# Kernel optimization log

Measured on AMD Instinct MI355X. Metric: run time of the kernel, lower is better.

## Reference

```python
import jax, jax.numpy as jnp
import numpy as np

N, E = 50000, 800000
D_IN, D_HID, D_OUT = 128, 128, 64
BN_EPS = 1e-5
GEN_EPS = 1e-7


def _lin_init(k, fan_in, shape):
    lim = 1.0 / np.sqrt(fan_in)
    return jax.random.uniform(k, shape, minval=-lim, maxval=lim, dtype=jnp.float32)


def setup_inputs() -> dict:
    key = jax.random.key(0)
    ks = jax.random.split(key, 12)
    x = jax.random.normal(ks[0], (N, D_IN), dtype=jnp.float32)
    edge_index = jax.random.randint(ks[1], (2, E), 0, N, dtype=jnp.int64)
    return {
        "x": x,
        # GCNConv 0 and 1 (Glorot-ish uniform init like PyG Linear)
        "W0": _lin_init(ks[2], D_IN, (D_IN, D_HID)), "b0": jnp.zeros((D_HID,), jnp.float32),
        "g0": jnp.ones((D_HID,), jnp.float32), "beta0": jnp.zeros((D_HID,), jnp.float32),
        "W1": _lin_init(ks[3], D_HID, (D_HID, D_HID)), "b1": jnp.zeros((D_HID,), jnp.float32),
        "g1": jnp.ones((D_HID,), jnp.float32), "beta1": jnp.zeros((D_HID,), jnp.float32),
        # GENConv MLP: [D_HID] -> [2*D_HID] (BN+ReLU) -> [D_OUT]
        "Wg1": _lin_init(ks[4], D_HID, (D_HID, 2 * D_HID)), "bg1": jnp.zeros((2 * D_HID,), jnp.float32),
        "gg": jnp.ones((2 * D_HID,), jnp.float32), "betag": jnp.zeros((2 * D_HID,), jnp.float32),
        "Wg2": _lin_init(ks[5], 2 * D_HID, (2 * D_HID, D_OUT)), "bg2": jnp.zeros((D_OUT,), jnp.float32),
        "edge_index": edge_index,
    }


def _bn(h, gamma, beta):
    # BatchNorm1d, training-mode batch statistics (biased variance)
    mu = jnp.mean(h, axis=0)
    var = jnp.mean(jnp.square(h - mu), axis=0)
    return (h - mu) * jax.lax.rsqrt(var + BN_EPS) * gamma + beta


def _gcn_conv(x, W, b, src, dst, n):
    # GCNConv: D^-1/2 (A + I) D^-1/2 (x W) + b
    loop = jnp.arange(n, dtype=src.dtype)
    s = jnp.concatenate([src, loop])
    d = jnp.concatenate([dst, loop])
    deg = jax.ops.segment_sum(jnp.ones_like(s, dtype=x.dtype), d, num_segments=n)
    dinv = jax.lax.rsqrt(deg)  # deg >= 1 due to self-loops
    norm = dinv[s] * dinv[d]   # [E+N]
    h = x @ W                  # [N, D]
    agg = jax.ops.segment_sum(norm[:, None] * h[s], d, num_segments=n)
    return agg + b


def _gen_conv(x, W1, b1, g, beta, W2, b2, src, dst, n):
    # GENConv (defaults): msg = relu(x_j) + eps; per-channel softmax aggregation
    # (t=1); residual add of x_dst; then MLP [D, 2D (BN+ReLU), D_out].
    msg = jax.nn.relu(x[src]) + GEN_EPS            # [E, D]
    m = jax.ops.segment_max(msg, dst, num_segments=n)
    m = jnp.where(jnp.isfinite(m), m, 0.0)         # guard zero in-degree nodes
    ex = jnp.exp(msg - m[dst])                     # [E, D]
    denom = jax.ops.segment_sum(ex, dst, num_segments=n)
    num = jax.ops.segment_sum(ex * msg, dst, num_segments=n)
    agg = num / jnp.maximum(denom, 1e-16)          # [N, D]
    out = agg + x                                  # residual
    h = jax.nn.relu(_bn(out @ W1 + b1, g, beta))
    return h @ W2 + b2


def reference(x, W0, b0, g0, beta0, W1, b1, g1, beta1,
              Wg1, bg1, gg, betag, Wg2, bg2, edge_index):
    src, dst = edge_index[0], edge_index[1]
    n = x.shape[0]
    # layer 0: GCNConv -> BN -> ReLU (dropout is identity in eval)
    h = _gcn_conv(x, W0, b0, src, dst, n)
    h = jax.nn.relu(_bn(h, g0, beta0))
    # layer 1
    h = _gcn_conv(h, W1, b1, src, dst, n)
    h = jax.nn.relu(_bn(h, g1, beta1))
    # final GENConv + log-softmax over classes
    h = _gen_conv(h, Wg1, bg1, gg, betag, Wg2, bg2, src, dst, n)
    return jax.nn.log_softmax(h, axis=-1)
```

## Files before the change

kernel.cpp:

```cpp
#include <hip/hip_runtime.h>
#include <hip/hip_bf16.h>

#define DIN 128
#define DHID 128
#define DCLS 64
#define BN_EPS 1e-5f
#define GEN_EPS 1e-7f

typedef __attribute__((ext_vector_type(8))) short short8;
typedef __attribute__((ext_vector_type(4))) float f32x4;

static __device__ __forceinline__ float bf2f(unsigned short u) {
    union { float f; unsigned int i; } x; x.i = ((unsigned int)u) << 16; return x.f;
}
static __device__ __forceinline__ unsigned short f2bf(float f) {
    union { float f; unsigned int i; } x; x.f = f;
    unsigned int r = x.i + 0x7fffu + ((x.i >> 16) & 1u);
    return (unsigned short)(r >> 16);
}
static __device__ __forceinline__ float bflo(unsigned int u) {
    union { float f; unsigned int i; } x; x.i = u << 16; return x.f;
}
static __device__ __forceinline__ float bfhi(unsigned int u) {
    union { float f; unsigned int i; } x; x.i = u & 0xffff0000u; return x.f;
}
static __device__ __forceinline__ unsigned int packbf(float lo, float hi) {
    return ((unsigned int)f2bf(hi) << 16) | f2bf(lo);
}

__global__ void k_hist(const int* __restrict__ dst, int* __restrict__ counts, int E) {
    int e = blockIdx.x * 256 + threadIdx.x;
    if (e < E) atomicAdd(&counts[dst[e]], 1);
}

__global__ __launch_bounds__(256) void k_scan1(const int* __restrict__ counts,
        int* __restrict__ roff, int* __restrict__ bsum, int N) {
    __shared__ int ls[256];
    int t = threadIdx.x;
    int base = blockIdx.x * 1024 + t * 4;
    int c0 = 0, c1 = 0, c2 = 0, c3 = 0;
    if (base + 3 < N) {
        int4 v = *(const int4*)(counts + base);
        c0 = v.x; c1 = v.y; c2 = v.z; c3 = v.w;
    } else {
        if (base + 0 < N) c0 = counts[base + 0];
        if (base + 1 < N) c1 = counts[base + 1];
        if (base + 2 < N) c2 = counts[base + 2];
        if (base + 3 < N) c3 = counts[base + 3];
    }
    ls[t] = c0 + c1 + c2 + c3;
    __syncthreads();
    for (int off = 1; off < 256; off <<= 1) {
        int v = (t >= off) ? ls[t - off] : 0;
        __syncthreads();
        ls[t] += v;
        __syncthreads();
    }
    int r = (t == 0) ? 0 : ls[t - 1];
    if (base + 0 < N) { roff[base + 0] = r; r += c0; }
    if (base + 1 < N) { roff[base + 1] = r; r += c1; }
    if (base + 2 < N) { roff[base + 2] = r; r += c2; }
    if (base + 3 < N) { roff[base + 3] = r; }
    if (t == 255) bsum[blockIdx.x] = ls[255];
}

__global__ void k_scan3(const int* __restrict__ counts, const int* __restrict__ bsum,
        int* __restrict__ roff, int* __restrict__ cursor, float* __restrict__ dinv,
        int N, int E) {
    __shared__ int sbase;
    if (threadIdx.x == 0) {
        int blk = (blockIdx.x * 256) >> 10;
        int s = 0;
        for (int j = 0; j < blk; j++) s += bsum[j];
        sbase = s;
    }
    __syncthreads();
    int i = blockIdx.x * 256 + threadIdx.x;
    if (i < N) {
        int r = roff[i] + sbase;
        roff[i] = r; cursor[i] = r;
        dinv[i] = rsqrtf((float)(counts[i] + 1));
    }
    if (i == 0) roff[N] = E;
}

__global__ void k_fill(const int* __restrict__ src, const int* __restrict__ dst,
        int* __restrict__ cursor, int* __restrict__ srcs, int E) {
    int e = blockIdx.x * 256 + threadIdx.x;
    if (e < E) {
        int d = dst[e];
        int p = atomicAdd(&cursor[d], 1);
        srcs[p] = src[e];
    }
}

__global__ void k_wt_all(const float* __restrict__ W0, const float* __restrict__ W1,
        const float* __restrict__ Wg1, const float* __restrict__ Wg2,
        unsigned short* __restrict__ w0t, unsigned short* __restrict__ w1t,
        unsigned short* __restrict__ wg1t, unsigned short* __restrict__ wg2t) {
    int i = blockIdx.x * 256 + threadIdx.x;
    const float* W; unsigned short* Wt; int Kk, Dd, j;
    if (i < 16384)      { W = W0;  Wt = w0t;  Kk = 128; Dd = 128; j = i; }
    else if (i < 32768) { W = W1;  Wt = w1t;  Kk = 128; Dd = 128; j = i - 16384; }
    else if (i < 65536) { W = Wg1; Wt = wg1t; Kk = 128; Dd = 256; j = i - 32768; }
    else if (i < 81920) { W = Wg2; Wt = wg2t; Kk = 256; Dd = 64;  j = i - 65536; }
    else return;
    int n = j / Kk, k = j - n * Kk;
    Wt[j] = f2bf(W[(size_t)k * Dd + n]);
}

template<int K, int CTILE, bool ABF16, bool OBF16, bool STATS, bool HEAD, bool SFIN>
__global__ __launch_bounds__(256) void k_gemm(const void* __restrict__ Av,
        const unsigned short* __restrict__ Wt, const float* __restrict__ bias,
        const float* __restrict__ bnsum, const float* __restrict__ bnsq,
        const float* __restrict__ bng, const float* __restrict__ bnbeta, float invN,
        const float* __restrict__ rowscale,
        void* __restrict__ Cv, float* __restrict__ gsum, float* __restrict__ gsq,
        int nrows, int Dout) {
    constexpr int KP = 136;
    constexpr int NF = CTILE / 32;
    constexpr int BNSZ = SFIN ? 2 * K : 2;
    __shared__ unsigned short smem[(64 + CTILE) * KP];
    __shared__ float sBN[BNSZ];
    unsigned short* sA = smem;
    unsigned short* sW = smem + 64 * KP;
    const int tid = threadIdx.x;
    const int row0 = blockIdx.x * 64, col0 = blockIdx.y * CTILE;

    if (SFIN) {
        for (int c = tid; c < K; c += 256) {
            float mu = bnsum[c] * invN;
            float var = bnsq[c] * invN - mu * mu;
            float s = bng[c] * rsqrtf(var + BN_EPS);
            sBN[c] = s; sBN[K + c] = bnbeta[c] - mu * s;
        }
        __syncthreads();
    }

    const int w = tid >> 6, lane = tid & 63;
    const int wr = (w >> 1) * 32, wc = (w & 1) * (CTILE / 2);
    const int lr = lane & 15, kg = (lane >> 4) * 8;
    f32x4 acc[2][NF] = {};

    for (int kh = 0; kh < K; kh += 128) {
#pragma unroll
        for (int it = 0; it < 8; ++it) {
            int idx = (it * 256 + tid) * 4;
            int r = idx >> 7, c = idx & 127;
            int gr = row0 + r;
            float v0 = 0.f, v1 = 0.f, v2 = 0.f, v3 = 0.f;
            if (gr < nrows) {
                if (ABF16) {
                    ushort4 u = *(const ushort4*)((const unsigned short*)Av + (size_t)gr * K + kh + c);
                    v0 = bf2f(u.x); v1 = bf2f(u.y); v2 = bf2f(u.z); v3 = bf2f(u.w);
                } else {
                    float4 f = *(const float4*)((const float*)Av + (size_t)gr * K + kh + c);
                    v0 = f.x; v1 = f.y; v2 = f.z; v3 = f.w;
                }
                if (SFIN) {
                    int cc = kh + c;
                    v0 = fmaxf(v0 * sBN[cc + 0] + sBN[K + cc + 0], 0.f);
                    v1 = fmaxf(v1 * sBN[cc + 1] + sBN[K + cc + 1], 0.f);
                    v2 = fmaxf(v2 * sBN[cc + 2] + sBN[K + cc + 2], 0.f);
                    v3 = fmaxf(v3 * sBN[cc + 3] + sBN[K + cc + 3], 0.f);
                }
            }
            ushort4 o; o.x = f2bf(v0); o.y = f2bf(v1); o.z = f2bf(v2); o.w = f2bf(v3);
            *(ushort4*)(&sA[r * KP + c]) = o;
        }
#pragma unroll
        for (int it = 0; it < (CTILE * 128) / (256 * 8); ++it) {
            int idx = (it * 256 + tid) * 8;
            int r = idx >> 7, c = idx & 127;
            uint4 u = *(const uint4*)(Wt + (size_t)(col0 + r) * K + kh + c);
            *(uint4*)(&sW[r * KP + c]) = u;
        }
        __syncthreads();
#pragma unroll
        for (int kk = 0; kk < 128; kk += 32) {
            short8 af[2], bfr[NF];
#pragma unroll
            for (int mi = 0; mi < 2; mi++)
                af[mi] = *(const short8*)(&sA[(wr + mi * 16 + lr) * KP + kk + kg]);
#pragma unroll
            for (int ni = 0; ni < NF; ni++)
                bfr[ni] = *(const short8*)(&sW[(wc + ni * 16 + lr) * KP + kk + kg]);
#pragma unroll
            for (int mi = 0; mi < 2; mi++)
#pragma unroll
                for (int ni = 0; ni < NF; ni++)
                    acc[mi][ni] = __builtin_amdgcn_mfma_f32_16x16x32_bf16(af[mi], bfr[ni], acc[mi][ni], 0, 0, 0);
        }
        __syncthreads();
    }

    float* fs = (float*)smem;
    if (STATS) {
        if (tid < 2 * CTILE) fs[tid] = 0.f;
        __syncthreads();
    }

    float stat_s[NF], stat_q[NF];
#pragma unroll
    for (int ni = 0; ni < NF; ni++) { stat_s[ni] = 0.f; stat_q[ni] = 0.f; }

#pragma unroll
    for (int mi = 0; mi < 2; mi++) {
#pragma unroll
        for (int ni = 0; ni < NF; ni++) {
            int r = wr + mi * 16 + (lane >> 4) * 4;
            int cloc = wc + ni * 16 + (lane & 15);
            int cgl = col0 + cloc;
            float bv = bias ? bias[cgl] : 0.f;
#pragma unroll
            for (int j = 0; j < 4; j++) {
                int gr = row0 + r + j;
                if (gr < nrows) {
                    float val = acc[mi][ni][j] + bv;
                    if (rowscale) val *= rowscale[gr];
                    if (STATS) { stat_s[ni] += val; stat_q[ni] += val * val; }
                    if (HEAD) {
                        fs[(r + j) * 65 + cloc] = val;
                    } else if (OBF16) {
                        ((unsigned short*)Cv)[(size_t)gr * Dout + cgl] = f2bf(val);
                    } else {
                        ((float*)Cv)[(size_t)gr * Dout + cgl] = val;
                    }
                } else if (HEAD) {
                    fs[(r + j) * 65 + cloc] = 0.f;
                }
            }
        }
    }

    if (STATS) {
#pragma unroll
        for (int ni = 0; ni < NF; ni++) {
            int cloc = wc + ni * 16 + (lane & 15);
            atomicAdd(&fs[cloc], stat_s[ni]);
            atomicAdd(&fs[CTILE + cloc], stat_q[ni]);
        }
        __syncthreads();
        if (tid < CTILE) {
            atomicAdd(&gsum[col0 + tid], fs[tid]);
            atomicAdd(&gsq[col0 + tid], fs[CTILE + tid]);
        }
    }

    if (HEAD) {
        __syncthreads();
        for (int rr = 0; rr < 16; rr++) {
            int row = w * 16 + rr;
            int gr = row0 + row;
            if (gr >= nrows) break;
            float v = fs[row * 65 + lane];
            float m = v;
            for (int o = 32; o; o >>= 1) m = fmaxf(m, __shfl_xor(m, o));
            float e = __expf(v - m);
            float s = e;
            for (int o = 32; o; o >>= 1) s += __shfl_xor(s, o);
            ((float*)Cv)[(size_t)gr * 64 + lane] = v - m - __logf(s);
        }
    }
}

#define ACC8(u) { a0 += bflo(u.x); a1 += bfhi(u.x); a2 += bflo(u.y); a3 += bfhi(u.y); \
                  a4 += bflo(u.z); a5 += bfhi(u.z); a6 += bflo(u.w); a7 += bfhi(u.w); }

__global__ __launch_bounds__(256) void k_gcn_agg(const unsigned short* __restrict__ p,
        const int* __restrict__ roff, const int* __restrict__ srcs,
        const float* __restrict__ dinv, const float* __restrict__ b,
        unsigned short* __restrict__ out,
        float* __restrict__ gsum, float* __restrict__ gsq, int N) {
    int nw = (gridDim.x * 256) >> 6;
    int wid = (blockIdx.x * 256 + threadIdx.x) >> 6;
    int lane = threadIdx.x & 63;
    int q = lane >> 4, l16 = lane & 15;
    int c = l16 * 8;
    float4 bl = *(const float4*)(b + c);
    float4 bh = *(const float4*)(b + c + 4);
    float bb[8] = {bl.x, bl.y, bl.z, bl.w, bh.x, bh.y, bh.z, bh.w};
    float ls[8] = {0,0,0,0,0,0,0,0};
    float lq[8] = {0,0,0,0,0,0,0,0};
    for (int d = wid; d < N; d += nw) {
        float a0=0.f,a1=0.f,a2=0.f,a3=0.f,a4=0.f,a5=0.f,a6=0.f,a7=0.f;
        int e0 = roff[d], e1 = roff[d + 1];
        for (int e = e0 + q; e < e1; e += 4) {
            int s = srcs[e];
            uint4 u = ((const uint4*)(p + (size_t)s * 128))[l16];
            ACC8(u);
        }
        if (q == 0) {
            uint4 u = ((const uint4*)(p + (size_t)d * 128))[l16];
            ACC8(u);
        }
        a0 += __shfl_xor(a0,16); a0 += __shfl_xor(a0,32);
        a1 += __shfl_xor(a1,16); a1 += __shfl_xor(a1,32);
        a2 += __shfl_xor(a2,16); a2 += __shfl_xor(a2,32);
        a3 += __shfl_xor(a3,16); a3 += __shfl_xor(a3,32);
        a4 += __shfl_xor(a4,16); a4 += __shfl_xor(a4,32);
        a5 += __shfl_xor(a5,16); a5 += __shfl_xor(a5,32);
        a6 += __shfl_xor(a6,16); a6 += __shfl_xor(a6,32);
        a7 += __shfl_xor(a7,16); a7 += __shfl_xor(a7,32);
        if (q == 0) {
            float dv = dinv[d];
            float r0 = dv*a0 + bb[0], r1 = dv*a1 + bb[1];
            float r2 = dv*a2 + bb[2], r3 = dv*a3 + bb[3];
            float r4 = dv*a4 + bb[4], r5 = dv*a5 + bb[5];
            float r6 = dv*a6 + bb[6], r7 = dv*a7 + bb[7];
            ls[0]+=r0; lq[0]+=r0*r0; ls[1]+=r1; lq[1]+=r1*r1;
            ls[2]+=r2; lq[2]+=r2*r2; ls[3]+=r3; lq[3]+=r3*r3;
            ls[4]+=r4; lq[4]+=r4*r4; ls[5]+=r5; lq[5]+=r5*r5;
            ls[6]+=r6; lq[6]+=r6*r6; ls[7]+=r7; lq[7]+=r7*r7;
            uint4 o;
            o.x = packbf(r0, r1); o.y = packbf(r2, r3);
            o.z = packbf(r4, r5); o.w = packbf(r6, r7);
            ((uint4*)(out + (size_t)d * 128))[l16] = o;
        }
    }
    __shared__ float sred[4][128];
    __shared__ float qred[4][128];
    int wv = threadIdx.x >> 6;
    if (q == 0) {
#pragma unroll
        for (int k = 0; k < 8; k++) { sred[wv][c + k] = ls[k]; qred[wv][c + k] = lq[k]; }
    }
    __syncthreads();
    int t = threadIdx.x;
    if (t < 128) {
        float s = sred[0][t] + sred[1][t] + sred[2][t] + sred[3][t];
        float qq = qred[0][t] + qred[1][t] + qred[2][t] + qred[3][t];
        atomicAdd(&gsum[t], s);
        atomicAdd(&gsq[t], qq);
    }
}

__global__ __launch_bounds__(256) void k_genpre(const unsigned short* __restrict__ t4,
        const float* __restrict__ bnsum, const float* __restrict__ bnsq,
        const float* __restrict__ bng, const float* __restrict__ bnbeta, float invN,
        unsigned short* __restrict__ wt, int N) {
    __shared__ float ssc[128], ssh[128];
    int tid = threadIdx.x;
    if (tid < 128) {
        float mu = bnsum[tid] * invN;
        float var = bnsq[tid] * invN - mu * mu;
        float s = bng[tid] * rsqrtf(var + BN_EPS);
        ssc[tid] = s; ssh[tid] = bnbeta[tid] - mu * s;
    }
    __syncthreads();
    int i = blockIdx.x * 256 + tid;
    int node = i >> 4, l16 = i & 15;
    if (node >= N) return;
    int c = l16 * 8;
    uint4 u = ((const uint4*)(t4 + (size_t)node * 128))[l16];
    float v[8] = {bflo(u.x), bfhi(u.x), bflo(u.y), bfhi(u.y),
                  bflo(u.z), bfhi(u.z), bflo(u.w), bfhi(u.w)};
    float w[8];
#pragma unroll
    for (int k = 0; k < 8; k++) {
        float m = fmaxf(v[k] * ssc[c + k] + ssh[c + k], 0.f) + GEN_EPS;
        m = fminf(m, 80.f);
        w[k] = __expf(m);
    }
    uint4 ow;
    ow.x = packbf(w[0], w[1]); ow.y = packbf(w[2], w[3]);
    ow.z = packbf(w[4], w[5]); ow.w = packbf(w[6], w[7]);
    ((uint4*)(wt + (size_t)node * 128))[l16] = ow;
}

__global__ __launch_bounds__(256) void k_gen_agg(const unsigned short* __restrict__ t4,
        const unsigned short* __restrict__ wt,
        const int* __restrict__ roff, const int* __restrict__ srcs,
        const float* __restrict__ bnsum, const float* __restrict__ bnsq,
        const float* __restrict__ bng, const float* __restrict__ bnbeta, float invN,
        unsigned short* __restrict__ out, int N) {
    __shared__ float ssc[128], ssh[128];
    int tid = threadIdx.x;
    if (tid < 128) {
        float mu = bnsum[tid] * invN;
        float var = bnsq[tid] * invN - mu * mu;
        float s = bng[tid] * rsqrtf(var + BN_EPS);
        ssc[tid] = s; ssh[tid] = bnbeta[tid] - mu * s;
    }
    __syncthreads();
    int nw = (gridDim.x * 256) >> 6;
    int wid = (blockIdx.x * 256 + tid) >> 6;
    int lane = tid & 63;
    int q = lane >> 4, l16 = lane & 15;
    int c = l16 * 8;
    for (int d = wid; d < N; d += nw) {
        float de[8] = {0,0,0,0,0,0,0,0};
        float nu[8] = {0,0,0,0,0,0,0,0};
        int e0 = roff[d], e1 = roff[d + 1];
        for (int e = e0 + q; e < e1; e += 4) {
            int s = srcs[e];
            uint4 u = ((const uint4*)(wt + (size_t)s * 128))[l16];
            float w0 = bflo(u.x), w1 = bfhi(u.x), w2 = bflo(u.y), w3 = bfhi(u.y);
            float w4 = bflo(u.z), w5 = bfhi(u.z), w6 = bflo(u.w), w7 = bfhi(u.w);
            de[0] += w0; nu[0] += w0 * __logf(w0);
            de[1] += w1; nu[1] += w1 * __logf(w1);
            de[2] += w2; nu[2] += w2 * __logf(w2);
            de[3] += w3; nu[3] += w3 * __logf(w3);
            de[4] += w4; nu[4] += w4 * __logf(w4);
            de[5] += w5; nu[5] += w5 * __logf(w5);
            de[6] += w6; nu[6] += w6 * __logf(w6);
            de[7] += w7; nu[7] += w7 * __logf(w7);
        }
#pragma unroll
        for (int k = 0; k < 8; k++) {
            de[k] += __shfl_xor(de[k],16); de[k] += __shfl_xor(de[k],32);
            nu[k] += __shfl_xor(nu[k],16); nu[k] += __shfl_xor(nu[k],32);
        }
        if (q == 0) {
            uint4 u = ((const uint4*)(t4 + (size_t)d * 128))[l16];
            float v[8] = {bflo(u.x), bfhi(u.x), bflo(u.y), bfhi(u.y),
                          bflo(u.z), bfhi(u.z), bflo(u.w), bfhi(u.w)};
            float r[8];
            bool has = (e1 > e0);
#pragma unroll
            for (int k = 0; k < 8; k++) {
                float h2 = fmaxf(v[k] * ssc[c + k] + ssh[c + k], 0.f);
                float a = has ? nu[k] / de[k] : 0.f;
                r[k] = a + h2;
            }
            uint4 o;
            o.x = packbf(r[0], r[1]); o.y = packbf(r[2], r[3]);
            o.z = packbf(r[4], r[5]); o.w = packbf(r[6], r[7]);
            ((uint4*)(out + (size_t)d * 128))[l16] = o;
        }
    }
}

extern "C" void kernel_launch(void* const* d_in, const int* in_sizes, int n_in,
                              void* d_out, int out_size, void* d_ws, size_t ws_size,
                              hipStream_t stream) {
    const float* x   = (const float*)d_in[0];
    const float* W0  = (const float*)d_in[1];
    const float* b0  = (const float*)d_in[2];
    const float* g0  = (const float*)d_in[3];
    const float* be0 = (const float*)d_in[4];
    const float* W1  = (const float*)d_in[5];
    const float* b1  = (const float*)d_in[6];
    const float* g1  = (const float*)d_in[7];
    const float* be1 = (const float*)d_in[8];
    const float* Wg1 = (const float*)d_in[9];
    const float* bg1 = (const float*)d_in[10];
    const float* gg  = (const float*)d_in[11];
    const float* beg = (const float*)d_in[12];
    const float* Wg2 = (const float*)d_in[13];
    const float* bg2 = (const float*)d_in[14];
    const int*   ei  = (const int*)d_in[15];

    const int N = in_sizes[0] / DIN;
    const int E = in_sizes[15] / 2;
    const int* src = ei;
    const int* dst = ei + E;

    char* ws = (char*)d_ws;
    size_t off = 0;
    auto alloc = [&](size_t b) { size_t o = off; off = (off + b + 255) & ~(size_t)255; return o; };
    size_t o_counts = alloc((size_t)N * 4);
    size_t o_stats  = alloc(1024 * 4);
    size_t o_cursor = alloc((size_t)N * 4);
    size_t o_roff   = alloc(((size_t)N + 1) * 4);
    size_t o_srcs   = alloc((size_t)E * 4);
    size_t o_dinv   = alloc((size_t)N * 4);
    size_t o_bsum   = alloc(1024 * 4);
    size_t o_w0t    = alloc(128 * 128 * 2);
    size_t o_w1t    = alloc(128 * 128 * 2);
    size_t o_wg1t   = alloc(256 * 128 * 2);
    size_t o_wg2t   = alloc(64 * 256 * 2);
    size_t o_xa     = alloc((size_t)N * 128 * 2);
    size_t o_xb     = alloc((size_t)N * 128 * 2);
    size_t o_c      = alloc((size_t)N * 256 * 2);
    (void)ws_size; (void)n_in; (void)out_size;

    int* counts = (int*)(ws + o_counts);
    float* stats = (float*)(ws + o_stats);
    int* cursor = (int*)(ws + o_cursor);
    int* roff = (int*)(ws + o_roff);
    int* srcs = (int*)(ws + o_srcs);
    float* dinv = (float*)(ws + o_dinv);
    int* bsum = (int*)(ws + o_bsum);
    unsigned short* w0t  = (unsigned short*)(ws + o_w0t);
    unsigned short* w1t  = (unsigned short*)(ws + o_w1t);
    unsigned short* wg1t = (unsigned short*)(ws + o_wg1t);
    unsigned short* wg2t = (unsigned short*)(ws + o_wg2t);
    unsigned short* xa = (unsigned short*)(ws + o_xa);
    unsigned short* xb = (unsigned short*)(ws + o_xb);
    unsigned short* cb = (unsigned short*)(ws + o_c);
    unsigned short* wtab = cb;

    float* sum0 = stats;       float* sq0 = stats + 128;
    float* sum1 = stats + 256; float* sq1 = stats + 384;
    float* sumg = stats + 512; float* sqg = stats + 768;

    hipMemsetAsync(ws + o_counts, 0, o_cursor - o_counts, stream);

    int egrid = (E + 255) / 256;
    int nblk = (N + 1023) / 1024;
    k_hist<<<egrid, 256, 0, stream>>>(dst, counts, E);
    k_scan1<<<nblk, 256, 0, stream>>>(counts, roff, bsum, N);
    k_scan3<<<(N + 255) / 256, 256, 0, stream>>>(counts, bsum, roff, cursor, dinv, N, E);
    k_fill<<<egrid, 256, 0, stream>>>(src, dst, cursor, srcs, E);

    k_wt_all<<<320, 256, 0, stream>>>(W0, W1, Wg1, Wg2, w0t, w1t, wg1t, wg2t);

    int rb = (N + 63) / 64;
    const float invN = 1.f / (float)N;

    k_gemm<128, 128, false, true, false, false, false><<<dim3(rb, 1), 256, 0, stream>>>(
        x, w0t, nullptr, nullptr, nullptr, nullptr, nullptr, 0.f, dinv, xa, nullptr, nullptr, N, 128);
    k_gcn_agg<<<2048, 256, 0, stream>>>(xa, roff, srcs, dinv, b0, xb, sum0, sq0, N);

    k_gemm<128, 128, true, true, false, false, true><<<dim3(rb, 1), 256, 0, stream>>>(
        xb, w1t, nullptr, sum0, sq0, g0, be0, invN, dinv, xa, nullptr, nullptr, N, 128);
    k_gcn_agg<<<2048, 256, 0, stream>>>(xa, roff, srcs, dinv, b1, xb, sum1, sq1, N);

    k_genpre<<<(N * 16 + 255) / 256, 256, 0, stream>>>(xb, sum1, sq1, g1, be1, invN, wtab, N);
    k_gen_agg<<<2048, 256, 0, stream>>>(xb, wtab, roff, srcs, sum1, sq1, g1, be1, invN, xa, N);

    k_gemm<128, 128, true, true, true, false, false><<<dim3(rb, 2), 256, 0, stream>>>(
        xa, wg1t, bg1, nullptr, nullptr, nullptr, nullptr, 0.f, nullptr, cb, sumg, sqg, N, 256);

    k_gemm<256, 64, true, false, false, true, true><<<dim3(rb, 1), 256, 0, stream>>>(
        cb, wg2t, bg2, sumg, sqg, gg, beg, invN, nullptr, d_out, nullptr, nullptr, N, 64);
}
```

Before: 489.3 us.

## Fuse CSR build into cooperative kernel and precompute softmax numerator table

Replaces the memset plus the histogram, two scan and fill kernels with one cooperative kernel that uses grid-wide syncs between phases. This removes several launches and the memset. The GEN preprocessing kernel now stores both exp(m) and exp(m)*m per node, so the aggregation loop no longer computes a log per edge element. That doubles the gathered bytes per edge in exchange for dropping that transcendental work. Grid syncs and the serial bsum scan on one thread add some latency.

```diff
diff --git a/kernel.cpp b/kernel.cpp
--- a/kernel.cpp
+++ b/kernel.cpp
@@ -1,5 +1,8 @@
 #include <hip/hip_runtime.h>
 #include <hip/hip_bf16.h>
+#include <hip/hip_cooperative_groups.h>
+
+namespace cg = cooperative_groups;
 
 #define DIN 128
 #define DHID 128
@@ -28,66 +31,62 @@
     return ((unsigned int)f2bf(hi) << 16) | f2bf(lo);
 }
 
-__global__ void k_hist(const int* __restrict__ dst, int* __restrict__ counts, int E) {
-    int e = blockIdx.x * 256 + threadIdx.x;
-    if (e < E) atomicAdd(&counts[dst[e]], 1);
-}
-
-__global__ __launch_bounds__(256) void k_scan1(const int* __restrict__ counts,
-        int* __restrict__ roff, int* __restrict__ bsum, int N) {
+__global__ __launch_bounds__(256) void k_csr(const int* __restrict__ src,
+        const int* __restrict__ dst, int* __restrict__ counts, int* __restrict__ cursor,
+        int* __restrict__ roff, int* __restrict__ bsum, int* __restrict__ srcs,
+        float* __restrict__ dinv, float* __restrict__ stats, int N, int E) {
+    cg::grid_group grid = cg::this_grid();
     __shared__ int ls[256];
-    int t = threadIdx.x;
-    int base = blockIdx.x * 1024 + t * 4;
-    int c0 = 0, c1 = 0, c2 = 0, c3 = 0;
-    if (base + 3 < N) {
-        int4 v = *(const int4*)(counts + base);
-        c0 = v.x; c1 = v.y; c2 = v.z; c3 = v.w;
-    } else {
-        if (base + 0 < N) c0 = counts[base + 0];
-        if (base + 1 < N) c1 = counts[base + 1];
-        if (base + 2 < N) c2 = counts[base + 2];
-        if (base + 3 < N) c3 = counts[base + 3];
-    }
-    ls[t] = c0 + c1 + c2 + c3;
-    __syncthreads();
-    for (int off = 1; off < 256; off <<= 1) {
-        int v = (t >= off) ? ls[t - off] : 0;
-        __syncthreads();
-        ls[t] += v;
-        __syncthreads();
-    }
-    int r = (t == 0) ? 0 : ls[t - 1];
-    if (base + 0 < N) { roff[base + 0] = r; r += c0; }
-    if (base + 1 < N) { roff[base + 1] = r; r += c1; }
-    if (base + 2 < N) { roff[base + 2] = r; r += c2; }
-    if (base + 3 < N) { roff[base + 3] = r; }
-    if (t == 255) bsum[blockIdx.x] = ls[255];
-}
-
-__global__ void k_scan3(const int* __restrict__ counts, const int* __restrict__ bsum,
-        int* __restrict__ roff, int* __restrict__ cursor, float* __restrict__ dinv,
-        int N, int E) {
-    __shared__ int sbase;
-    if (threadIdx.x == 0) {
-        int blk = (blockIdx.x * 256) >> 10;
-        int s = 0;
-        for (int j = 0; j < blk; j++) s += bsum[j];
-        sbase = s;
-    }
-    __syncthreads();
-    int i = blockIdx.x * 256 + threadIdx.x;
-    if (i < N) {
-        int r = roff[i] + sbase;
+    const int gsz = gridDim.x * 256;
+    const int gtid = blockIdx.x * 256 + threadIdx.x;
+    for (int i = gtid; i < N; i += gsz) counts[i] = 0;
+    if (gtid < 1024) stats[gtid] = 0.f;
+    grid.sync();
+    for (int e = gtid; e < E; e += gsz) atomicAdd(&counts[dst[e]], 1);
+    grid.sync();
+    int nblk = (N + 1023) >> 10;
+    if ((int)blockIdx.x < nblk) {
+        int t = threadIdx.x;
+        int base = blockIdx.x * 1024 + t * 4;
+        int c0 = 0, c1 = 0, c2 = 0, c3 = 0;
+        if (base + 3 < N) {
+            int4 v = *(const int4*)(counts + base);
+            c0 = v.x; c1 = v.y; c2 = v.z; c3 = v.w;
+        } else {
+            if (base + 0 < N) c0 = counts[base + 0];
+            if (base + 1 < N) c1 = counts[base + 1];
+            if (base + 2 < N) c2 = counts[base + 2];
+            if (base + 3 < N) c3 = counts[base + 3];
+        }
+        ls[t] = c0 + c1 + c2 + c3;
+        __syncthreads();
+        for (int off = 1; off < 256; off <<= 1) {
+            int v = (t >= off) ? ls[t - off] : 0;
+            __syncthreads();
+            ls[t] += v;
+            __syncthreads();
+        }
+        int r = (t == 0) ? 0 : ls[t - 1];
+        if (base + 0 < N) { roff[base + 0] = r; r += c0; }
+        if (base + 1 < N) { roff[base + 1] = r; r += c1; }
+        if (base + 2 < N) { roff[base + 2] = r; r += c2; }
+        if (base + 3 < N) { roff[base + 3] = r; }
+        if (t == 255) bsum[blockIdx.x] = ls[255];
+    }
+    grid.sync();
+    if (gtid == 0) {
+        int run = 0;
+        for (int j = 0; j < nblk; j++) { int v = bsum[j]; bsum[j] = run; run += v; }
+    }
+    grid.sync();
+    for (int i = gtid; i < N; i += gsz) {
+        int r = roff[i] + bsum[i >> 10];
         roff[i] = r; cursor[i] = r;
         dinv[i] = rsqrtf((float)(counts[i] + 1));
     }
-    if (i == 0) roff[N] = E;
-}
-
-__global__ void k_fill(const int* __restrict__ src, const int* __restrict__ dst,
-        int* __restrict__ cursor, int* __restrict__ srcs, int E) {
-    int e = blockIdx.x * 256 + threadIdx.x;
-    if (e < E) {
+    if (gtid == 0) roff[N] = E;
+    grid.sync();
+    for (int e = gtid; e < E; e += gsz) {
         int d = dst[e];
         int p = atomicAdd(&cursor[d], 1);
         srcs[p] = src[e];
@@ -355,17 +354,22 @@
     uint4 u = ((const uint4*)(t4 + (size_t)node * 128))[l16];
     float v[8] = {bflo(u.x), bfhi(u.x), bflo(u.y), bfhi(u.y),
                   bflo(u.z), bfhi(u.z), bflo(u.w), bfhi(u.w)};
-    float w[8];
+    float w[8], wm[8];
 #pragma unroll
     for (int k = 0; k < 8; k++) {
         float m = fmaxf(v[k] * ssc[c + k] + ssh[c + k], 0.f) + GEN_EPS;
         m = fminf(m, 80.f);
         w[k] = __expf(m);
-    }
-    uint4 ow;
+        wm[k] = w[k] * m;
+    }
+    uint4* row = (uint4*)(wt + (size_t)node * 256);
+    uint4 ow, om;
     ow.x = packbf(w[0], w[1]); ow.y = packbf(w[2], w[3]);
     ow.z = packbf(w[4], w[5]); ow.w = packbf(w[6], w[7]);
-    ((uint4*)(wt + (size_t)node * 128))[l16] = ow;
+    om.x = packbf(wm[0], wm[1]); om.y = packbf(wm[2], wm[3]);
+    om.z = packbf(wm[4], wm[5]); om.w = packbf(wm[6], wm[7]);
+    row[l16] = ow;
+    row[16 + l16] = om;
 }
 
 __global__ __launch_bounds__(256) void k_gen_agg(const unsigned short* __restrict__ t4,
@@ -394,17 +398,17 @@
         int e0 = roff[d], e1 = roff[d + 1];
         for (int e = e0 + q; e < e1; e += 4) {
             int s = srcs[e];
-            uint4 u = ((const uint4*)(wt + (size_t)s * 128))[l16];
-            float w0 = bflo(u.x), w1 = bfhi(u.x), w2 = bflo(u.y), w3 = bfhi(u.y);
-            float w4 = bflo(u.z), w5 = bfhi(u.z), w6 = bflo(u.w), w7 = bfhi(u.w);
-            de[0] += w0; nu[0] += w0 * __logf(w0);
-            de[1] += w1; nu[1] += w1 * __logf(w1);
-            de[2] += w2; nu[2] += w2 * __logf(w2);
-            de[3] += w3; nu[3] += w3 * __logf(w3);
-            de[4] += w4; nu[4] += w4 * __logf(w4);
-            de[5] += w5; nu[5] += w5 * __logf(w5);
-            de[6] += w6; nu[6] += w6 * __logf(w6);
-            de[7] += w7; nu[7] += w7 * __logf(w7);
+            const uint4* row = (const uint4*)(wt + (size_t)s * 256);
+            uint4 uw = row[l16];
+            uint4 um = row[16 + l16];
+            de[0] += bflo(uw.x); de[1] += bfhi(uw.x);
+            de[2] += bflo(uw.y); de[3] += bfhi(uw.y);
+            de[4] += bflo(uw.z); de[5] += bfhi(uw.z);
+            de[6] += bflo(uw.w); de[7] += bfhi(uw.w);
+            nu[0] += bflo(um.x); nu[1] += bfhi(um.x);
+            nu[2] += bflo(um.y); nu[3] += bfhi(um.y);
+            nu[4] += bflo(um.z); nu[5] += bfhi(um.z);
+            nu[6] += bflo(um.w); nu[7] += bfhi(um.w);
         }
 #pragma unroll
         for (int k = 0; k < 8; k++) {
@@ -453,8 +457,8 @@
 
     const int N = in_sizes[0] / DIN;
     const int E = in_sizes[15] / 2;
-    const int* src = ei;
-    const int* dst = ei + E;
+    const int* srce = ei;
+    const int* dste = ei + E;
 
     char* ws = (char*)d_ws;
     size_t off = 0;
@@ -495,14 +499,13 @@
     float* sum1 = stats + 256; float* sq1 = stats + 384;
     float* sumg = stats + 512; float* sqg = stats + 768;
 
-    hipMemsetAsync(ws + o_counts, 0, o_cursor - o_counts, stream);
-
-    int egrid = (E + 255) / 256;
-    int nblk = (N + 1023) / 1024;
-    k_hist<<<egrid, 256, 0, stream>>>(dst, counts, E);
-    k_scan1<<<nblk, 256, 0, stream>>>(counts, roff, bsum, N);
-    k_scan3<<<(N + 255) / 256, 256, 0, stream>>>(counts, bsum, roff, cursor, dinv, N, E);
-    k_fill<<<egrid, 256, 0, stream>>>(src, dst, cursor, srcs, E);
+    {
+        int NPeople = N, EE = E;
+        void* args[] = { (void*)&srce, (void*)&dste, (void*)&counts, (void*)&cursor,
+                         (void*)&roff, (void*)&bsum, (void*)&srcs, (void*)&dinv,
+                         (void*)&stats, (void*)&NPeople, (void*)&EE };
+        hipLaunchCooperativeKernel((void*)k_csr, dim3(1024), dim3(256), args, 0, stream);
+    }
 
     k_wt_all<<<320, 256, 0, stream>>>(W0, W1, Wg1, Wg2, w0t, w1t, wg1t, wg2t);
 
```

After: 934.9 us. 91.1% more time.
